# Kernel tuning notes

Hardware: AMD Instinct MI355X
Metric: run time of the kernel (lower is better)

## Reference

```python
import jax, jax.numpy as jnp
import numpy as np

D_MODEL = 1024
N_HEAD = 16
D_HEAD = D_MODEL // N_HEAD
D_FF = 4096
B, S = 2, 2048
EPS = 1e-5


def setup_inputs() -> dict:
    key = jax.random.key(0)
    ks = jax.random.split(key, 16)
    sc = 1.0 / np.sqrt(D_MODEL)
    x = jax.random.normal(ks[0], (B, S, D_MODEL), dtype=jnp.float32)
    # causal mask: 1 where attention is disallowed (upper triangle)
    mask = jnp.triu(jnp.ones((S, S), dtype=jnp.int32), k=1)[None, None]
    p = {
        'x': x,
        'mask': mask,
        'wq': jax.random.normal(ks[1], (D_MODEL, D_MODEL), jnp.float32) * sc,
        'bq': jnp.zeros((D_MODEL,), jnp.float32),
        'wk': jax.random.normal(ks[2], (D_MODEL, D_MODEL), jnp.float32) * sc,
        'bk': jnp.zeros((D_MODEL,), jnp.float32),
        'wv': jax.random.normal(ks[3], (D_MODEL, D_MODEL), jnp.float32) * sc,
        'bv': jnp.zeros((D_MODEL,), jnp.float32),
        'wo': jax.random.normal(ks[4], (D_MODEL, D_MODEL), jnp.float32) * sc,
        'bo': jnp.zeros((D_MODEL,), jnp.float32),
        'w1': jax.random.normal(ks[5], (D_MODEL, D_FF), jnp.float32) * sc,
        'b1': jnp.zeros((D_FF,), jnp.float32),
        'w2': jax.random.normal(ks[6], (D_FF, D_MODEL), jnp.float32) * (1.0 / np.sqrt(D_FF)),
        'b2': jnp.zeros((D_MODEL,), jnp.float32),
        'g1': jnp.ones((D_MODEL,), jnp.float32),
        'beta1': jnp.zeros((D_MODEL,), jnp.float32),
        'g2': jnp.ones((D_MODEL,), jnp.float32),
        'beta2': jnp.zeros((D_MODEL,), jnp.float32),
    }
    return p


def _layer_norm(x, g, b):
    mu = jnp.mean(x, axis=-1, keepdims=True)
    var = jnp.mean(jnp.square(x - mu), axis=-1, keepdims=True)
    return (x - mu) * jax.lax.rsqrt(var + EPS) * g + b


def reference(x, mask, wq, bq, wk, bk, wv, bv, wo, bo, w1, b1, w2, b2, g1, beta1, g2, beta2):
    b, s, _ = x.shape
    # QKV projections -> [B, H, S, Dh]
    q = (x @ wq + bq).reshape(b, s, N_HEAD, D_HEAD).transpose(0, 2, 1, 3)
    k = (x @ wk + bk).reshape(b, s, N_HEAD, D_HEAD).transpose(0, 2, 1, 3)
    v = (x @ wv + bv).reshape(b, s, N_HEAD, D_HEAD).transpose(0, 2, 1, 3)
    scores = jnp.einsum('bhqd,bhkd->bhqk', q, k) / np.sqrt(D_HEAD)  # [B,H,S,S]
    scores = jnp.where(mask == 1, -jnp.inf, scores)
    attn = jax.nn.softmax(scores, axis=-1)
    out = jnp.einsum('bhqk,bhkd->bhqd', attn, v)
    out = out.transpose(0, 2, 1, 3).reshape(b, s, D_MODEL)
    attn_out = out @ wo + bo
    x1 = _layer_norm(x + attn_out, g1, beta1)
    ffn = jax.nn.relu(x1 @ w1 + b1) @ w2 + b2
    return _layer_norm(x1 + ffn, g2, beta2)
```

## Files before the change

kernel.cpp:

```cpp
#include <hip/hip_runtime.h>
#include <hip/hip_bf16.h>
#include <cstdint>

#define D_MODEL 1024
#define D_FF    4096
#define NHEAD   16
#define DHEAD   64
#define BATCH   2
#define SEQ     2048
#define BT      (BATCH*SEQ)
#define QKVLD   (3*D_MODEL)
#define LN_EPS  1e-5f

typedef __bf16 bf16_t;
typedef bf16_t bf16x8 __attribute__((ext_vector_type(8)));
typedef float  f32x4  __attribute__((ext_vector_type(4)));

__device__ __forceinline__ unsigned short f2b(float f){
  bf16_t h = (bf16_t)f;
  return __builtin_bit_cast(unsigned short, h);
}

__device__ __forceinline__ void gload16(const void* g, void* l){
  __builtin_amdgcn_global_load_lds(
      (const __attribute__((address_space(1))) unsigned int*)g,
      (__attribute__((address_space(3))) unsigned int*)l, 16, 0, 0);
}

__global__ __launch_bounds__(256) void cvt_f32_bf16(
    const float* __restrict__ in, unsigned short* __restrict__ out, int n){
  int i = (blockIdx.x*256 + threadIdx.x)*4;
  if (i < n){
    float4 v = *(const float4*)(in + i);
    ushort4 u; u.x=f2b(v.x); u.y=f2b(v.y); u.z=f2b(v.z); u.w=f2b(v.w);
    *(ushort4*)(out + i) = u;
  }
}

__global__ __launch_bounds__(256) void concat_bias(
    const float* __restrict__ bq, const float* __restrict__ bk,
    const float* __restrict__ bv, float* __restrict__ o){
  int i = blockIdx.x*256 + threadIdx.x;
  if (i < D_MODEL){ o[i]=bq[i]; o[D_MODEL+i]=bk[i]; o[2*D_MODEL+i]=bv[i]; }
}

__global__ __launch_bounds__(256) void transpose_cvt(
    const float* __restrict__ in, unsigned short* __restrict__ out, int R, int C){
  __shared__ float t[32][33];
  int c0 = blockIdx.x*32, r0 = blockIdx.y*32;
  int tx = threadIdx.x, ty = threadIdx.y;
  #pragma unroll
  for (int i=0;i<4;++i){ int r = ty + i*8; t[r][tx] = in[(size_t)(r0+r)*C + c0+tx]; }
  __syncthreads();
  #pragma unroll
  for (int i=0;i<4;++i){ int r = ty + i*8; out[(size_t)(c0+r)*R + r0+tx] = f2b(t[tx][r]); }
}

__global__ __launch_bounds__(256) void transpose_v(
    const unsigned short* __restrict__ QKV, unsigned short* __restrict__ Vt){
  __shared__ unsigned short t[32][33];
  int s0 = blockIdx.x*32, d0 = blockIdx.y*32, bh = blockIdx.z;
  int b = bh>>4, h = bh&15;
  int tx = threadIdx.x, ty = threadIdx.y;
  #pragma unroll
  for (int i=0;i<4;++i){ int r = ty + i*8;
    t[r][tx] = QKV[(size_t)(b*SEQ + s0+r)*QKVLD + 2*D_MODEL + h*DHEAD + d0+tx]; }
  __syncthreads();
  #pragma unroll
  for (int i=0;i<4;++i){ int r = ty + i*8;
    Vt[((size_t)bh*DHEAD + d0+r)*SEQ + s0+tx] = t[tx][r]; }
}

template<int EPI>
__global__ __launch_bounds__(512,4) void gemm128(
    const unsigned short* __restrict__ A, const unsigned short* __restrict__ Bt,
    const float* __restrict__ bias, const float* __restrict__ resid,
    float* __restrict__ outF, unsigned short* __restrict__ outB,
    int M, int N, int K){
  __shared__ __attribute__((aligned(16))) unsigned short As[2][128*64];
  __shared__ __attribute__((aligned(16))) unsigned short Bs[2][128*64];
  int tid = threadIdx.x;
  int lane = tid & 63, wave = tid >> 6;
  int lr = lane & 15, lg = lane >> 4;
  int row0 = blockIdx.x*128, col0 = blockIdx.y*128;
  int wr = (wave>>2)*64, wc = (wave&3)*32;
  int x7 = lr & 7;

  int sr = tid >> 3;
  int sl = (tid & 7) ^ (sr & 7);
  auto STAGE = [&](int k0, int buf){
    #pragma unroll
    for (int it=0; it<2; ++it){
      int c = it*512 + tid;
      int r = it*64 + sr;
      gload16(A  + (size_t)(row0+r)*K + k0 + sl*8, &As[buf][c<<3]);
      gload16(Bt + (size_t)(col0+r)*K + k0 + sl*8, &Bs[buf][c<<3]);
    }
  };

  f32x4 acc[4][2] = {};
  int nk = K >> 6;
  STAGE(0, 0);
  int cur = 0;
  for (int t=0; t<nk; ++t){
    if (t+1 < nk){
      STAGE((t+1)<<6, cur^1);
      asm volatile("s_waitcnt vmcnt(4)" ::: "memory");
    } else {
      asm volatile("s_waitcnt vmcnt(0)" ::: "memory");
    }
    __builtin_amdgcn_s_barrier();
    #pragma unroll
    for (int kk=0; kk<2; ++kk){
      int sk = ((kk*4 + lg) ^ x7) << 3;
      bf16x8 af[4], bfr[2];
      #pragma unroll
      for (int mi=0;mi<4;++mi) af[mi]  = *(const bf16x8*)&As[cur][(wr+mi*16+lr)*64 + sk];
      #pragma unroll
      for (int ni=0;ni<2;++ni) bfr[ni] = *(const bf16x8*)&Bs[cur][(wc+ni*16+lr)*64 + sk];
      #pragma unroll
      for (int mi=0;mi<4;++mi)
        #pragma unroll
        for (int ni=0;ni<2;++ni)
          acc[mi][ni] = __builtin_amdgcn_mfma_f32_16x16x32_bf16(af[mi], bfr[ni], acc[mi][ni], 0,0,0);
    }
    __builtin_amdgcn_s_barrier();
    cur ^= 1;
  }
  #pragma unroll
  for (int mi=0;mi<4;++mi){
    int row = row0 + wr + mi*16 + (lg<<2);
    #pragma unroll
    for (int ni=0;ni<2;++ni){
      int col = col0 + wc + ni*16 + lr;
      float bs = bias[col];
      #pragma unroll
      for (int j=0;j<4;++j){
        size_t idx = (size_t)(row+j)*N + col;
        float v = acc[mi][ni][j] + bs;
        if (EPI==1){ v += resid[idx]; outF[idx] = v; }
        else if (EPI==2){ v = fmaxf(v, 0.f); outB[idx] = f2b(v); }
        else { outB[idx] = f2b(v); }
      }
    }
  }
}

__global__ __launch_bounds__(256,2) void attn_k(
    const unsigned short* __restrict__ QKV,
    const unsigned short* __restrict__ Vt, unsigned short* __restrict__ O){
  __shared__ __attribute__((aligned(16))) unsigned short Ks[2][128*64];
  __shared__ __attribute__((aligned(16))) unsigned short Vs[2][64*128];
  __shared__ __attribute__((aligned(16))) unsigned short Ps[4][16*128];
  int tid = threadIdx.x, lane = tid&63, wave = tid>>6;
  int lr = lane&15, lg = lane>>4;
  int bid = blockIdx.x;
  int L = (bid & 7)*64 + (bid >> 3);
  int qx = L & 15;
  int bh = L >> 4;
  int b = bh>>4, h = bh&15;
  const int NT = SEQ/64;

  #pragma unroll 1
  for (int half=0; half<2; ++half){
    int qt = half ? qx : (NT-1 - qx);
    int q0w = qt*64 + wave*16;

    const unsigned short* Qrow = QKV + (size_t)(b*SEQ + q0w + lr)*QKVLD + h*DHEAD;
    bf16x8 qf[2];
    qf[0] = *(const bf16x8*)(Qrow + lg*8);
    qf[1] = *(const bf16x8*)(Qrow + 32 + lg*8);

    f32x4 oacc[4] = {};
    float m_run[4], l_run[4];
    #pragma unroll
    for (int j=0;j<4;++j){ m_run[j] = -1e30f; l_run[j] = 0.f; }

    auto STAGE = [&](int t, int buf){
      int kv0 = t*128;
      #pragma unroll
      for (int it=0; it<4; ++it){
        int c = it*256 + tid;
        int rk = c>>3, slk = (c&7) ^ (rk&7);
        gload16(QKV + (size_t)(b*SEQ + kv0 + rk)*QKVLD + D_MODEL + h*DHEAD + slk*8, &Ks[buf][c<<3]);
        int rv = c>>4, slv = (c&15) ^ (rv&15);
        gload16(Vt + ((size_t)bh*DHEAD + rv)*SEQ + kv0 + slv*8, &Vs[buf][c<<3]);
      }
    };

    int nkv = (qt + 2) >> 1;
    STAGE(0, 0);
    int cur = 0;
    for (int t=0; t<nkv; ++t){
      if (t+1 < nkv){
        STAGE(t+1, cur^1);
        asm volatile("s_waitcnt vmcnt(8)" ::: "memory");
      } else {
        asm volatile("s_waitcnt vmcnt(0)" ::: "memory");
      }
      __builtin_amdgcn_s_barrier();

      int kv0 = t*128;
      f32x4 sacc[8] = {};
      #pragma unroll
      for (int kk=0;kk<2;++kk){
        #pragma unroll
        for (int ni=0;ni<8;++ni){
          int krow = ni*16 + lr;
          bf16x8 kf = *(const bf16x8*)&Ks[cur][krow*64 + (((kk*4+lg) ^ (krow&7))<<3)];
          sacc[ni] = __builtin_amdgcn_mfma_f32_16x16x32_bf16(qf[kk], kf, sacc[ni], 0,0,0);
        }
      }
      if (t == nkv-1){
        #pragma unroll
        for (int ni=0;ni<8;++ni){
          f32x4 v = sacc[ni];
          int kpos = kv0 + ni*16 + lr;
          #pragma unroll
          for (int j=0;j<4;++j){
            int qpos = q0w + lg*4 + j;
            float sv = v[j]*0.125f;
            v[j] = (kpos > qpos) ? -1e30f : sv;
          }
          sacc[ni] = v;
        }
      } else {
        #pragma unroll
        for (int ni=0;ni<8;++ni) sacc[ni] *= 0.125f;
      }
      #pragma unroll
      for (int j=0;j<4;++j){
        float rm = -1e30f;
        #pragma unroll
        for (int ni=0;ni<8;++ni) rm = fmaxf(rm, sacc[ni][j]);
        #pragma unroll
        for (int d=1; d<16; d<<=1) rm = fmaxf(rm, __shfl_xor(rm, d, 16));
        float mnew = fmaxf(m_run[j], rm);
        float corr = __expf(m_run[j] - mnew);
        m_run[j] = mnew;
        float rs_ = 0.f;
        #pragma unroll
        for (int ni=0;ni<8;++ni){
          float p = __expf(sacc[ni][j] - mnew);
          sacc[ni][j] = p;
          rs_ += p;
        }
        #pragma unroll
        for (int d=1; d<16; d<<=1) rs_ += __shfl_xor(rs_, d, 16);
        l_run[j] = l_run[j]*corr + rs_;
        #pragma unroll
        for (int nd=0; nd<4; ++nd) oacc[nd][j] *= corr;
      }
      #pragma unroll
      for (int ni=0;ni<8;++ni)
        #pragma unroll
        for (int j=0;j<4;++j){
          int qrow = lg*4 + j;
          int kcol = ni*16 + lr;
          int slot = (kcol>>3) ^ (qrow&15);
          Ps[wave][qrow*128 + slot*8 + (kcol&7)] = f2b(sacc[ni][j]);
        }
      #pragma unroll
      for (int kk=0;kk<4;++kk){
        bf16x8 pa = *(const bf16x8*)&Ps[wave][lr*128 + (((kk*4+lg) ^ (lr&15))<<3)];
        #pragma unroll
        for (int nd=0; nd<4; ++nd){
          int dr = nd*16 + lr;
          bf16x8 vf = *(const bf16x8*)&Vs[cur][dr*128 + (((kk*4+lg) ^ (dr&15))<<3)];
          oacc[nd] = __builtin_amdgcn_mfma_f32_16x16x32_bf16(pa, vf, oacc[nd], 0,0,0);
        }
      }
      __builtin_amdgcn_s_barrier();
      cur ^= 1;
    }
    #pragma unroll
    for (int j=0;j<4;++j){
      float inv = 1.f / l_run[j];
      int token = b*SEQ + q0w + lg*4 + j;
      #pragma unroll
      for (int nd=0; nd<4; ++nd)
        O[(size_t)token*D_MODEL + h*DHEAD + nd*16 + lr] = f2b(oacc[nd][j]*inv);
    }
  }
}

template<int MODE>
__global__ __launch_bounds__(256) void ln_k(
    const float* __restrict__ in, const float* __restrict__ g, const float* __restrict__ bta,
    float* __restrict__ outF, unsigned short* __restrict__ outB){
  int row = blockIdx.x, tid = threadIdx.x;
  float4 v = ((const float4*)(in + (size_t)row*D_MODEL))[tid];
  float s = v.x+v.y+v.z+v.w;
  float q = v.x*v.x+v.y*v.y+v.z*v.z+v.w*v.w;
  #pragma unroll
  for (int d=32; d; d>>=1){ s += __shfl_xor(s, d); q += __shfl_xor(q, d); }
  __shared__ float rs[4], rq[4];
  int wave = tid>>6;
  if ((tid&63)==0){ rs[wave]=s; rq[wave]=q; }
  __syncthreads();
  s = rs[0]+rs[1]+rs[2]+rs[3];
  q = rq[0]+rq[1]+rq[2]+rq[3];
  float mu  = s * (1.f/D_MODEL);
  float var = q * (1.f/D_MODEL) - mu*mu;
  float rstd = rsqrtf(var + LN_EPS);
  float4 gg = ((const float4*)g)[tid];
  float4 bb = ((const float4*)bta)[tid];
  float o0 = (v.x-mu)*rstd*gg.x + bb.x;
  float o1 = (v.y-mu)*rstd*gg.y + bb.y;
  float o2 = (v.z-mu)*rstd*gg.z + bb.z;
  float o3 = (v.w-mu)*rstd*gg.w + bb.w;
  float4 o; o.x=o0; o.y=o1; o.z=o2; o.w=o3;
  ((float4*)(outF + (size_t)row*D_MODEL))[tid] = o;
  if (MODE==0){
    ushort4 u; u.x=f2b(o0); u.y=f2b(o1); u.z=f2b(o2); u.w=f2b(o3);
    ((ushort4*)(outB + (size_t)row*D_MODEL))[tid] = u;
  }
}

extern "C" void kernel_launch(void* const* d_in, const int* in_sizes, int n_in,
                              void* d_out, int out_size, void* d_ws, size_t ws_size,
                              hipStream_t stream){
  const float* x  = (const float*)d_in[0];
  const float* wq = (const float*)d_in[2];  const float* bq = (const float*)d_in[3];
  const float* wk = (const float*)d_in[4];  const float* bk = (const float*)d_in[5];
  const float* wv = (const float*)d_in[6];  const float* bv = (const float*)d_in[7];
  const float* wo = (const float*)d_in[8];  const float* bo = (const float*)d_in[9];
  const float* w1 = (const float*)d_in[10]; const float* b1 = (const float*)d_in[11];
  const float* w2 = (const float*)d_in[12]; const float* b2 = (const float*)d_in[13];
  const float* g1 = (const float*)d_in[14]; const float* be1= (const float*)d_in[15];
  const float* g2 = (const float*)d_in[16]; const float* be2= (const float*)d_in[17];

  char* w = (char*)d_ws;
  size_t off = 0;
  auto nxt = [&](size_t bytes)->void*{
    void* p = w + off; off = (off + bytes + 255) & ~(size_t)255; return p;
  };
  unsigned short* xb    = (unsigned short*)nxt((size_t)BT*D_MODEL*2);
  unsigned short* wqkvT = (unsigned short*)nxt((size_t)QKVLD*D_MODEL*2);
  unsigned short* woT   = (unsigned short*)nxt((size_t)D_MODEL*D_MODEL*2);
  unsigned short* w1T   = (unsigned short*)nxt((size_t)D_MODEL*D_FF*2);
  unsigned short* w2T   = (unsigned short*)nxt((size_t)D_MODEL*D_FF*2);
  float*          bqkv  = (float*)nxt((size_t)QKVLD*4);
  unsigned short* QKV   = (unsigned short*)nxt((size_t)BT*QKVLD*2);
  unsigned short* VtG   = (unsigned short*)nxt((size_t)BT*D_MODEL*2);
  unsigned short* attnb = (unsigned short*)nxt((size_t)BT*D_MODEL*2);
  float*          hbuf  = (float*)nxt((size_t)BT*D_MODEL*4);
  float*          x1f   = (float*)nxt((size_t)BT*D_MODEL*4);
  unsigned short* ffn1  = (unsigned short*)nxt((size_t)BT*D_FF*2);
  unsigned short* x1b   = attnb;
  float*          h2    = hbuf;

  dim3 tb(32,8);
  cvt_f32_bf16<<<(BT*D_MODEL)/1024, 256, 0, stream>>>(x, xb, BT*D_MODEL);
  concat_bias<<<4, 256, 0, stream>>>(bq, bk, bv, bqkv);
  transpose_cvt<<<dim3(D_MODEL/32, D_MODEL/32), tb, 0, stream>>>(wq, wqkvT,                    D_MODEL, D_MODEL);
  transpose_cvt<<<dim3(D_MODEL/32, D_MODEL/32), tb, 0, stream>>>(wk, wqkvT + D_MODEL*D_MODEL,  D_MODEL, D_MODEL);
  transpose_cvt<<<dim3(D_MODEL/32, D_MODEL/32), tb, 0, stream>>>(wv, wqkvT + 2*D_MODEL*D_MODEL,D_MODEL, D_MODEL);
  transpose_cvt<<<dim3(D_MODEL/32, D_MODEL/32), tb, 0, stream>>>(wo, woT, D_MODEL, D_MODEL);
  transpose_cvt<<<dim3(D_FF/32,    D_MODEL/32), tb, 0, stream>>>(w1, w1T, D_MODEL, D_FF);
  transpose_cvt<<<dim3(D_MODEL/32, D_FF/32),    tb, 0, stream>>>(w2, w2T, D_FF, D_MODEL);

  gemm128<0><<<dim3(BT/128, QKVLD/128), 512, 0, stream>>>(xb, wqkvT, bqkv, nullptr, nullptr, QKV, BT, QKVLD, D_MODEL);

  transpose_v<<<dim3(SEQ/32, DHEAD/32, BATCH*NHEAD), tb, 0, stream>>>(QKV, VtG);
  attn_k<<<512, 256, 0, stream>>>(QKV, VtG, attnb);

  gemm128<1><<<dim3(BT/128, D_MODEL/128), 512, 0, stream>>>(attnb, woT, bo, x, hbuf, nullptr, BT, D_MODEL, D_MODEL);
  ln_k<0><<<BT, 256, 0, stream>>>(hbuf, g1, be1, x1f, x1b);
  gemm128<2><<<dim3(BT/128, D_FF/128), 512, 0, stream>>>(x1b, w1T, b1, nullptr, nullptr, ffn1, BT, D_FF, D_MODEL);
  gemm128<1><<<dim3(BT/128, D_MODEL/128), 512, 0, stream>>>(ffn1, w2T, b2, x1f, h2, nullptr, BT, D_MODEL, D_FF);
  ln_k<1><<<BT, 256, 0, stream>>>(h2, g2, be2, (float*)d_out, nullptr);
}
```

Before: 253.5 us.

## Single-buffer attention tiles, one q-tile per block, raise occupancy with setprio

The attention kernel drops K/V double buffering to cut LDS use and raises launch bounds from 2 to 3 blocks per CU. Each block now handles one query tile, with heavy tiles scheduled first, instead of a paired heavy/light tile, so the grid doubles to 1024 blocks. s_setprio is raised around the MFMA sections so waves in the matrix phase get issue priority. In exchange, loads are no longer overlapped with compute inside a block, so latency hiding depends on other resident blocks.

```diff
diff --git a/kernel.cpp b/kernel.cpp
--- a/kernel.cpp
+++ b/kernel.cpp
@@ -146,141 +146,133 @@
   }
 }
 
-__global__ __launch_bounds__(256,2) void attn_k(
+__global__ __launch_bounds__(256,3) void attn_k(
     const unsigned short* __restrict__ QKV,
     const unsigned short* __restrict__ Vt, unsigned short* __restrict__ O){
-  __shared__ __attribute__((aligned(16))) unsigned short Ks[2][128*64];
-  __shared__ __attribute__((aligned(16))) unsigned short Vs[2][64*128];
+  __shared__ __attribute__((aligned(16))) unsigned short Ks[128*64];
+  __shared__ __attribute__((aligned(16))) unsigned short Vs[64*128];
   __shared__ __attribute__((aligned(16))) unsigned short Ps[4][16*128];
   int tid = threadIdx.x, lane = tid&63, wave = tid>>6;
   int lr = lane&15, lg = lane>>4;
   int bid = blockIdx.x;
-  int L = (bid & 7)*64 + (bid >> 3);
-  int qx = L & 15;
-  int bh = L >> 4;
+  int L = (bid & 7)*128 + (bid >> 3);
+  int bh = L >> 5;
+  int qrank = L & 31;
+  int qt = 31 - qrank;
   int b = bh>>4, h = bh&15;
-  const int NT = SEQ/64;
-
-  #pragma unroll 1
-  for (int half=0; half<2; ++half){
-    int qt = half ? qx : (NT-1 - qx);
-    int q0w = qt*64 + wave*16;
-
-    const unsigned short* Qrow = QKV + (size_t)(b*SEQ + q0w + lr)*QKVLD + h*DHEAD;
-    bf16x8 qf[2];
-    qf[0] = *(const bf16x8*)(Qrow + lg*8);
-    qf[1] = *(const bf16x8*)(Qrow + 32 + lg*8);
-
-    f32x4 oacc[4] = {};
-    float m_run[4], l_run[4];
-    #pragma unroll
-    for (int j=0;j<4;++j){ m_run[j] = -1e30f; l_run[j] = 0.f; }
-
-    auto STAGE = [&](int t, int buf){
-      int kv0 = t*128;
-      #pragma unroll
-      for (int it=0; it<4; ++it){
-        int c = it*256 + tid;
-        int rk = c>>3, slk = (c&7) ^ (rk&7);
-        gload16(QKV + (size_t)(b*SEQ + kv0 + rk)*QKVLD + D_MODEL + h*DHEAD + slk*8, &Ks[buf][c<<3]);
-        int rv = c>>4, slv = (c&15) ^ (rv&15);
-        gload16(Vt + ((size_t)bh*DHEAD + rv)*SEQ + kv0 + slv*8, &Vs[buf][c<<3]);
-      }
-    };
-
-    int nkv = (qt + 2) >> 1;
-    STAGE(0, 0);
-    int cur = 0;
-    for (int t=0; t<nkv; ++t){
-      if (t+1 < nkv){
-        STAGE(t+1, cur^1);
-        asm volatile("s_waitcnt vmcnt(8)" ::: "memory");
-      } else {
-        asm volatile("s_waitcnt vmcnt(0)" ::: "memory");
-      }
-      __builtin_amdgcn_s_barrier();
-
-      int kv0 = t*128;
-      f32x4 sacc[8] = {};
-      #pragma unroll
-      for (int kk=0;kk<2;++kk){
-        #pragma unroll
-        for (int ni=0;ni<8;++ni){
-          int krow = ni*16 + lr;
-          bf16x8 kf = *(const bf16x8*)&Ks[cur][krow*64 + (((kk*4+lg) ^ (krow&7))<<3)];
-          sacc[ni] = __builtin_amdgcn_mfma_f32_16x16x32_bf16(qf[kk], kf, sacc[ni], 0,0,0);
-        }
-      }
-      if (t == nkv-1){
-        #pragma unroll
-        for (int ni=0;ni<8;++ni){
-          f32x4 v = sacc[ni];
-          int kpos = kv0 + ni*16 + lr;
-          #pragma unroll
-          for (int j=0;j<4;++j){
-            int qpos = q0w + lg*4 + j;
-            float sv = v[j]*0.125f;
-            v[j] = (kpos > qpos) ? -1e30f : sv;
-          }
-          sacc[ni] = v;
-        }
-      } else {
-        #pragma unroll
-        for (int ni=0;ni<8;++ni) sacc[ni] *= 0.125f;
-      }
-      #pragma unroll
-      for (int j=0;j<4;++j){
-        float rm = -1e30f;
-        #pragma unroll
-        for (int ni=0;ni<8;++ni) rm = fmaxf(rm, sacc[ni][j]);
-        #pragma unroll
-        for (int d=1; d<16; d<<=1) rm = fmaxf(rm, __shfl_xor(rm, d, 16));
-        float mnew = fmaxf(m_run[j], rm);
-        float corr = __expf(m_run[j] - mnew);
-        m_run[j] = mnew;
-        float rs_ = 0.f;
-        #pragma unroll
-        for (int ni=0;ni<8;++ni){
-          float p = __expf(sacc[ni][j] - mnew);
-          sacc[ni][j] = p;
-          rs_ += p;
-        }
-        #pragma unroll
-        for (int d=1; d<16; d<<=1) rs_ += __shfl_xor(rs_, d, 16);
-        l_run[j] = l_run[j]*corr + rs_;
-        #pragma unroll
-        for (int nd=0; nd<4; ++nd) oacc[nd][j] *= corr;
-      }
-      #pragma unroll
-      for (int ni=0;ni<8;++ni)
+  int q0w = qt*64 + wave*16;
+
+  const unsigned short* Qrow = QKV + (size_t)(b*SEQ + q0w + lr)*QKVLD + h*DHEAD;
+  bf16x8 qf[2];
+  qf[0] = *(const bf16x8*)(Qrow + lg*8);
+  qf[1] = *(const bf16x8*)(Qrow + 32 + lg*8);
+
+  f32x4 oacc[4] = {};
+  float m_run[4], l_run[4];
+  #pragma unroll
+  for (int j=0;j<4;++j){ m_run[j] = -1e30f; l_run[j] = 0.f; }
+
+  auto STAGE = [&](int t){
+    int kv0 = t*128;
+    #pragma unroll
+    for (int it=0; it<4; ++it){
+      int c = it*256 + tid;
+      int rk = c>>3, slk = (c&7) ^ (rk&7);
+      gload16(QKV + (size_t)(b*SEQ + kv0 + rk)*QKVLD + D_MODEL + h*DHEAD + slk*8, &Ks[c<<3]);
+      int rv = c>>4, slv = (c&15) ^ (rv&15);
+      gload16(Vt + ((size_t)bh*DHEAD + rv)*SEQ + kv0 + slv*8, &Vs[c<<3]);
+    }
+  };
+
+  int nkv = (qt + 2) >> 1;
+  for (int t=0; t<nkv; ++t){
+    STAGE(t);
+    asm volatile("s_waitcnt vmcnt(0)" ::: "memory");
+    __builtin_amdgcn_s_barrier();
+
+    int kv0 = t*128;
+    f32x4 sacc[8] = {};
+    __builtin_amdgcn_s_setprio(1);
+    #pragma unroll
+    for (int kk=0;kk<2;++kk){
+      #pragma unroll
+      for (int ni=0;ni<8;++ni){
+        int krow = ni*16 + lr;
+        bf16x8 kf = *(const bf16x8*)&Ks[krow*64 + (((kk*4+lg) ^ (krow&7))<<3)];
+        sacc[ni] = __builtin_amdgcn_mfma_f32_16x16x32_bf16(qf[kk], kf, sacc[ni], 0,0,0);
+      }
+    }
+    __builtin_amdgcn_s_setprio(0);
+    if (t == nkv-1){
+      #pragma unroll
+      for (int ni=0;ni<8;++ni){
+        f32x4 v = sacc[ni];
+        int kpos = kv0 + ni*16 + lr;
         #pragma unroll
         for (int j=0;j<4;++j){
-          int qrow = lg*4 + j;
-          int kcol = ni*16 + lr;
-          int slot = (kcol>>3) ^ (qrow&15);
-          Ps[wave][qrow*128 + slot*8 + (kcol&7)] = f2b(sacc[ni][j]);
+          int qpos = q0w + lg*4 + j;
+          float sv = v[j]*0.125f;
+          v[j] = (kpos > qpos) ? -1e30f : sv;
         }
-      #pragma unroll
-      for (int kk=0;kk<4;++kk){
-        bf16x8 pa = *(const bf16x8*)&Ps[wave][lr*128 + (((kk*4+lg) ^ (lr&15))<<3)];
-        #pragma unroll
-        for (int nd=0; nd<4; ++nd){
-          int dr = nd*16 + lr;
-          bf16x8 vf = *(const bf16x8*)&Vs[cur][dr*128 + (((kk*4+lg) ^ (dr&15))<<3)];
-          oacc[nd] = __builtin_amdgcn_mfma_f32_16x16x32_bf16(pa, vf, oacc[nd], 0,0,0);
-        }
-      }
-      __builtin_amdgcn_s_barrier();
-      cur ^= 1;
+        sacc[ni] = v;
+      }
+    } else {
+      #pragma unroll
+      for (int ni=0;ni<8;++ni) sacc[ni] *= 0.125f;
     }
     #pragma unroll
     for (int j=0;j<4;++j){
-      float inv = 1.f / l_run[j];
-      int token = b*SEQ + q0w + lg*4 + j;
-      #pragma unroll
-      for (int nd=0; nd<4; ++nd)
-        O[(size_t)token*D_MODEL + h*DHEAD + nd*16 + lr] = f2b(oacc[nd][j]*inv);
-    }
+      float rm = -1e30f;
+      #pragma unroll
+      for (int ni=0;ni<8;++ni) rm = fmaxf(rm, sacc[ni][j]);
+      #pragma unroll
+      for (int d=1; d<16; d<<=1) rm = fmaxf(rm, __shfl_xor(rm, d, 16));
+      float mnew = fmaxf(m_run[j], rm);
+      float corr = __expf(m_run[j] - mnew);
+      m_run[j] = mnew;
+      float rs_ = 0.f;
+      #pragma unroll
+      for (int ni=0;ni<8;++ni){
+        float p = __expf(sacc[ni][j] - mnew);
+        sacc[ni][j] = p;
+        rs_ += p;
+      }
+      #pragma unroll
+      for (int d=1; d<16; d<<=1) rs_ += __shfl_xor(rs_, d, 16);
+      l_run[j] = l_run[j]*corr + rs_;
+      #pragma unroll
+      for (int nd=0; nd<4; ++nd) oacc[nd][j] *= corr;
+    }
+    #pragma unroll
+    for (int ni=0;ni<8;++ni)
+      #pragma unroll
+      for (int j=0;j<4;++j){
+        int qrow = lg*4 + j;
+        int kcol = ni*16 + lr;
+        int slot = (kcol>>3) ^ (qrow&15);
+        Ps[wave][qrow*128 + slot*8 + (kcol&7)] = f2b(sacc[ni][j]);
+      }
+    __builtin_amdgcn_s_setprio(1);
+    #pragma unroll
+    for (int kk=0;kk<4;++kk){
+      bf16x8 pa = *(const bf16x8*)&Ps[wave][lr*128 + (((kk*4+lg) ^ (lr&15))<<3)];
+      #pragma unroll
+      for (int nd=0; nd<4; ++nd){
+        int dr = nd*16 + lr;
+        bf16x8 vf = *(const bf16x8*)&Vs[dr*128 + (((kk*4+lg) ^ (dr&15))<<3)];
+        oacc[nd] = __builtin_amdgcn_mfma_f32_16x16x32_bf16(pa, vf, oacc[nd], 0,0,0);
+      }
+    }
+    __builtin_amdgcn_s_setprio(0);
+    __builtin_amdgcn_s_barrier();
+  }
+  #pragma unroll
+  for (int j=0;j<4;++j){
+    float inv = 1.f / l_run[j];
+    int token = b*SEQ + q0w + lg*4 + j;
+    #pragma unroll
+    for (int nd=0; nd<4; ++nd)
+      O[(size_t)token*D_MODEL + h*DHEAD + nd*16 + lr] = f2b(oacc[nd][j]*inv);
   }
 }
 
@@ -363,7 +355,7 @@
   gemm128<0><<<dim3(BT/128, QKVLD/128), 512, 0, stream>>>(xb, wqkvT, bqkv, nullptr, nullptr, QKV, BT, QKVLD, D_MODEL);
 
   transpose_v<<<dim3(SEQ/32, DHEAD/32, BATCH*NHEAD), tb, 0, stream>>>(QKV, VtG);
-  attn_k<<<512, 256, 0, stream>>>(QKV, VtG, attnb);
+  attn_k<<<1024, 256, 0, stream>>>(QKV, VtG, attnb);
 
   gemm128<1><<<dim3(BT/128, D_MODEL/128), 512, 0, stream>>>(attnb, woT, bo, x, hbuf, nullptr, BT, D_MODEL, D_MODEL);
   ln_k<0><<<BT, 256, 0, stream>>>(hbuf, g1, be1, x1f, x1b);
```

Result: slower. 263.3 us (+3.9%).
